# Kernel tuning notes

Measured on AMD Instinct MI355X. Metric: run time of the kernel, lower is better.

The kernel has to match this reference:

```python
import jax, jax.numpy as jnp
import numpy as np

B, S, D = 64, 512, 768   # docs, bert seq len, bert hidden
E = 32                   # entities per doc
N_ENT = B * E            # 2048 global entity segments
MPE = 4                  # mentions per entity
M = N_ENT * MPE          # 8192 flat mentions
N_TYPES = 6
P = B * E * (E - 1)      # 63488 ordered pairs (h != t), per all_possible_pair


def setup_inputs() -> dict:
    key = jax.random.key(0)
    k1, k2, k3 = jax.random.split(key, 3)
    hidden = jax.random.normal(k1, (B, S, D), dtype=jnp.float32)
    # every entity has exactly MPE mentions -> no empty segments
    mention_entity = (jnp.arange(M, dtype=jnp.int32) // MPE)
    # positions indexed at pos+1 in the original, so keep pos in [0, S-1)
    mention_pos = jax.random.randint(k2, (M,), 0, S - 1, dtype=jnp.int32)
    # all ordered pairs h != t within each doc (all_possible_pair semantics)
    idx = np.arange(E)
    hh, tt = np.meshgrid(idx, idx, indexing='ij')
    mask = hh != tt
    hh, tt = hh[mask], tt[mask]              # [E*(E-1)]
    doc = np.repeat(np.arange(B), hh.size)   # [P]
    pair_head = jnp.asarray(doc * E + np.tile(hh, B), dtype=jnp.int32)
    pair_tail = jnp.asarray(doc * E + np.tile(tt, B), dtype=jnp.int32)
    pair_doc = jnp.asarray(doc, dtype=jnp.int32)
    ent_type = jax.random.randint(k3, (N_ENT,), 0, N_TYPES, dtype=jnp.int32)
    return {
        'hidden': hidden,
        'mention_entity': mention_entity,
        'mention_pos': mention_pos,
        'pair_head': pair_head,
        'pair_tail': pair_tail,
        'pair_doc': pair_doc,
        'ent_type': ent_type,
    }


def reference(hidden, mention_entity, mention_pos, pair_head, pair_tail, pair_doc, ent_type):
    # --- aggregate_entities: ragged per-entity logsumexp over mention tokens ---
    mention_doc = mention_entity // E                      # [M]
    m_emb = hidden[mention_doc, mention_pos + 1]           # [M, D] gather (pos[0]+1)
    seg_max = jax.ops.segment_max(m_emb, mention_entity, num_segments=N_ENT)  # [N_ENT, D]
    ent = jnp.log(
        jax.ops.segment_sum(jnp.exp(m_emb - seg_max[mention_entity]),
                            mention_entity, num_segments=N_ENT)
    ) + seg_max                                            # [N_ENT, D] stable logsumexp
    # --- extract_feature: per-pair stack of [cls, ent_h, ent_t] ---
    cls = hidden[:, 0]                                     # [B, D]
    feature_set = jnp.stack(
        [cls[pair_doc], ent[pair_head], ent[pair_tail]], axis=1)  # [P, 3, D]
    # --- pair type features: one_hot(..., 6).sum over the (h, t) pair ---
    types_oh = jax.nn.one_hot(ent_type, N_TYPES, dtype=jnp.float32)  # [N_ENT, 6]
    pair_types = types_oh[pair_head] + types_oh[pair_tail]           # [P, 6]
    return feature_set, pair_types
```

## Files before the change

### kernel.cpp

```cpp
#include <hip/hip_runtime.h>

#define B 64
#define S 512
#define D 768
#define E 32
#define N_ENT (B * E)
#define MPE 4
#define M (N_ENT * MPE)
#define N_TYPES 6
#define P (B * E * (E - 1))

#define D4 (D / 4)
#define LSE_THREADS (N_ENT * D4)
#define LSE_BLOCKS (LSE_THREADS / 256)
#define TYPES_ELEMS (P * N_TYPES)
#define TYPES_BLOCKS ((TYPES_ELEMS + 255) / 256)
#define FEAT_SLOTS (P * 3 * D4)

typedef float f32x4 __attribute__((ext_vector_type(4)));

__device__ __forceinline__ float lse4(float a, float b, float c, float d) {
    float mx = fmaxf(fmaxf(a, b), fmaxf(c, d));
    return logf(expf(a - mx) + expf(b - mx) + expf(c - mx) + expf(d - mx)) + mx;
}

__global__ __launch_bounds__(256) void prep_kernel(
    const float* __restrict__ hidden,
    const int* __restrict__ mention_entity,
    const int* __restrict__ mention_pos,
    const int* __restrict__ pair_head,
    const int* __restrict__ pair_tail,
    const int* __restrict__ ent_type,
    float* __restrict__ ent,
    float* __restrict__ out_types) {
    const unsigned b = blockIdx.x;
    const unsigned t = threadIdx.x;

    if (b < LSE_BLOCKS) {
        const unsigned idx = b * 256u + t;
        const unsigned e = idx / D4;
        const unsigned d4 = idx - e * D4;
        const int doc = mention_entity[e * MPE] / E;
        const float* rowbase = hidden + (size_t)doc * S * D + (size_t)d4 * 4;

        f32x4 x[MPE];
#pragma unroll
        for (int m = 0; m < MPE; ++m) {
            const int pos = mention_pos[e * MPE + m] + 1;
            x[m] = *(const f32x4*)(rowbase + (size_t)pos * D);
        }
        f32x4 o;
        o.x = lse4(x[0].x, x[1].x, x[2].x, x[3].x);
        o.y = lse4(x[0].y, x[1].y, x[2].y, x[3].y);
        o.z = lse4(x[0].z, x[1].z, x[2].z, x[3].z);
        o.w = lse4(x[0].w, x[1].w, x[2].w, x[3].w);
        *(f32x4*)(ent + (size_t)e * D + (size_t)d4 * 4) = o;
    } else {
        const unsigned i = (b - LSE_BLOCKS) * 256u + t;
        if (i < TYPES_ELEMS) {
            const unsigned p = i / N_TYPES;
            const int ty = (int)(i - p * N_TYPES);
            const int th = ent_type[pair_head[p]];
            const int tt = ent_type[pair_tail[p]];
            out_types[i] = (float)((ty == th) + (ty == tt));
        }
    }
}

__global__ __launch_bounds__(256) void feat_kernel(
    const float* __restrict__ hidden,
    const int* __restrict__ pair_head,
    const int* __restrict__ pair_tail,
    const int* __restrict__ pair_doc,
    const float* __restrict__ ent,
    f32x4* __restrict__ out4) {
    const unsigned stride = gridDim.x * blockDim.x;
    for (unsigned idx = blockIdx.x * blockDim.x + threadIdx.x;
         idx < (unsigned)FEAT_SLOTS; idx += stride) {
        const unsigned p = idx / (3 * D4);
        const unsigned rem = idx - p * (3 * D4);
        const unsigned r = rem / D4;
        const unsigned d4 = rem - r * D4;

        const f32x4* src;
        if (r == 0) {
            src = (const f32x4*)(hidden + (size_t)pair_doc[p] * (S * D));
        } else {
            const int q = (r == 1) ? pair_head[p] : pair_tail[p];
            src = (const f32x4*)(ent + (size_t)q * D);
        }
        __builtin_nontemporal_store(src[d4], &out4[idx]);
    }
}

extern "C" void kernel_launch(void* const* d_in, const int* in_sizes, int n_in,
                              void* d_out, int out_size, void* d_ws, size_t ws_size,
                              hipStream_t stream) {
    const float* hidden       = (const float*)d_in[0];
    const int* mention_entity = (const int*)d_in[1];
    const int* mention_pos    = (const int*)d_in[2];
    const int* pair_head      = (const int*)d_in[3];
    const int* pair_tail      = (const int*)d_in[4];
    const int* pair_doc       = (const int*)d_in[5];
    const int* ent_type       = (const int*)d_in[6];

    float* out       = (float*)d_out;
    float* out_feat  = out;
    float* out_types = out + (size_t)P * 3 * D;

    float* ent = (float*)d_ws;

    prep_kernel<<<LSE_BLOCKS + TYPES_BLOCKS, 256, 0, stream>>>(
        hidden, mention_entity, mention_pos, pair_head, pair_tail, ent_type,
        ent, out_types);

    feat_kernel<<<2048, 256, 0, stream>>>(
        hidden, pair_head, pair_tail, pair_doc, ent, (f32x4*)out_feat);
}
```

Measured before the change: 104.0 us.

## Move CLS row copy into prep kernel to overlap with entity logsumexp

Splits the feature-writing work so the CLS slice of each pair row, which does not depend on entity embeddings, is written by extra blocks in the first kernel alongside the logsumexp and type work. The second kernel then writes only the head and tail entity slices. The aim is to move about a third of the output traffic earlier so it overlaps with the prep phase and shortens the dependent second kernel. Writes now land in strided sub-rows rather than fully contiguous 3*D rows, which may reduce store coalescing at row boundaries.

```diff
diff --git a/kernel.cpp b/kernel.cpp
--- a/kernel.cpp
+++ b/kernel.cpp
@@ -11,11 +11,13 @@
 #define P (B * E * (E - 1))
 
 #define D4 (D / 4)
-#define LSE_THREADS (N_ENT * D4)
-#define LSE_BLOCKS (LSE_THREADS / 256)
+#define LSE_BLOCKS (N_ENT * D4 / 256)
 #define TYPES_ELEMS (P * N_TYPES)
 #define TYPES_BLOCKS ((TYPES_ELEMS + 255) / 256)
-#define FEAT_SLOTS (P * 3 * D4)
+#define CLS_BASE (LSE_BLOCKS + TYPES_BLOCKS)
+#define CLS_GRID 2048
+#define CLS_SLOTS (P * D4)
+#define HT_SLOTS (P * 2 * D4)
 
 typedef float f32x4 __attribute__((ext_vector_type(4)));
 
@@ -24,14 +26,16 @@
     return logf(expf(a - mx) + expf(b - mx) + expf(c - mx) + expf(d - mx)) + mx;
 }
 
-__global__ __launch_bounds__(256) void prep_kernel(
+__global__ __launch_bounds__(256) void prep_cls_kernel(
     const float* __restrict__ hidden,
     const int* __restrict__ mention_entity,
     const int* __restrict__ mention_pos,
     const int* __restrict__ pair_head,
     const int* __restrict__ pair_tail,
+    const int* __restrict__ pair_doc,
     const int* __restrict__ ent_type,
     float* __restrict__ ent,
+    float* __restrict__ out_feat,
     float* __restrict__ out_types) {
     const unsigned b = blockIdx.x;
     const unsigned t = threadIdx.x;
@@ -55,7 +59,7 @@
         o.z = lse4(x[0].z, x[1].z, x[2].z, x[3].z);
         o.w = lse4(x[0].w, x[1].w, x[2].w, x[3].w);
         *(f32x4*)(ent + (size_t)e * D + (size_t)d4 * 4) = o;
-    } else {
+    } else if (b < CLS_BASE) {
         const unsigned i = (b - LSE_BLOCKS) * 256u + t;
         if (i < TYPES_ELEMS) {
             const unsigned p = i / N_TYPES;
@@ -64,32 +68,35 @@
             const int tt = ent_type[pair_tail[p]];
             out_types[i] = (float)((ty == th) + (ty == tt));
         }
+    } else {
+        f32x4* out4 = (f32x4*)out_feat;
+        const unsigned stride = CLS_GRID * 256u;
+        for (unsigned idx = (b - CLS_BASE) * 256u + t; idx < (unsigned)CLS_SLOTS;
+             idx += stride) {
+            const unsigned p = idx / D4;
+            const unsigned d4 = idx - p * D4;
+            const f32x4* src = (const f32x4*)(hidden + (size_t)pair_doc[p] * (S * D));
+            __builtin_nontemporal_store(src[d4], &out4[(size_t)p * (3 * D4) + d4]);
+        }
     }
 }
 
-__global__ __launch_bounds__(256) void feat_kernel(
-    const float* __restrict__ hidden,
+__global__ __launch_bounds__(256) void ht_kernel(
     const int* __restrict__ pair_head,
     const int* __restrict__ pair_tail,
-    const int* __restrict__ pair_doc,
     const float* __restrict__ ent,
     f32x4* __restrict__ out4) {
     const unsigned stride = gridDim.x * blockDim.x;
     for (unsigned idx = blockIdx.x * blockDim.x + threadIdx.x;
-         idx < (unsigned)FEAT_SLOTS; idx += stride) {
-        const unsigned p = idx / (3 * D4);
-        const unsigned rem = idx - p * (3 * D4);
+         idx < (unsigned)HT_SLOTS; idx += stride) {
+        const unsigned p = idx / (2 * D4);
+        const unsigned rem = idx - p * (2 * D4);
         const unsigned r = rem / D4;
         const unsigned d4 = rem - r * D4;
-
-        const f32x4* src;
-        if (r == 0) {
-            src = (const f32x4*)(hidden + (size_t)pair_doc[p] * (S * D));
-        } else {
-            const int q = (r == 1) ? pair_head[p] : pair_tail[p];
-            src = (const f32x4*)(ent + (size_t)q * D);
-        }
-        __builtin_nontemporal_store(src[d4], &out4[idx]);
+        const int q = (r == 0) ? pair_head[p] : pair_tail[p];
+        const f32x4* src = (const f32x4*)(ent + (size_t)q * D);
+        __builtin_nontemporal_store(
+            src[d4], &out4[(size_t)p * (3 * D4) + (size_t)(r + 1) * D4 + d4]);
     }
 }
 
@@ -110,10 +117,10 @@
 
     float* ent = (float*)d_ws;
 
-    prep_kernel<<<LSE_BLOCKS + TYPES_BLOCKS, 256, 0, stream>>>(
-        hidden, mention_entity, mention_pos, pair_head, pair_tail, ent_type,
-        ent, out_types);
+    prep_cls_kernel<<<CLS_BASE + CLS_GRID, 256, 0, stream>>>(
+        hidden, mention_entity, mention_pos, pair_head, pair_tail, pair_doc,
+        ent_type, ent, out_feat, out_types);
 
-    feat_kernel<<<2048, 256, 0, stream>>>(
-        hidden, pair_head, pair_tail, pair_doc, ent, (f32x4*)out_feat);
+    ht_kernel<<<2048, 256, 0, stream>>>(
+        pair_head, pair_tail, ent, (f32x4*)out_feat);
 }
```

New measurement: 116.2 us. 1.12x slower.

## Fuse entity logsumexp into pair feature kernel, recomputing per pair

Applied to the files above, without the earlier changes.

Merges the prep and feature kernels into one launch. Each pair slot now recomputes the entity logsumexp from the gathered mention rows instead of reading a precomputed ent buffer, and type features are spread across the same grid. This removes a kernel launch and the ent workspace round trip. In exchange, each entity's logsumexp is recomputed about 62 times, adding many exp/log operations and gathered loads to a store-bound loop.

```diff
diff --git a/kernel.cpp b/kernel.cpp
--- a/kernel.cpp
+++ b/kernel.cpp
@@ -11,11 +11,10 @@
 #define P (B * E * (E - 1))
 
 #define D4 (D / 4)
-#define LSE_THREADS (N_ENT * D4)
-#define LSE_BLOCKS (LSE_THREADS / 256)
+#define FEAT_SLOTS (P * 3 * D4)
+#define GRID 2048
 #define TYPES_ELEMS (P * N_TYPES)
-#define TYPES_BLOCKS ((TYPES_ELEMS + 255) / 256)
-#define FEAT_SLOTS (P * 3 * D4)
+#define TYPES_PER_BLOCK ((TYPES_ELEMS + GRID - 1) / GRID)
 
 typedef float f32x4 __attribute__((ext_vector_type(4)));
 
@@ -24,40 +23,22 @@
     return logf(expf(a - mx) + expf(b - mx) + expf(c - mx) + expf(d - mx)) + mx;
 }
 
-__global__ __launch_bounds__(256) void prep_kernel(
+__global__ __launch_bounds__(256) void fused_kernel(
     const float* __restrict__ hidden,
     const int* __restrict__ mention_entity,
     const int* __restrict__ mention_pos,
     const int* __restrict__ pair_head,
     const int* __restrict__ pair_tail,
+    const int* __restrict__ pair_doc,
     const int* __restrict__ ent_type,
-    float* __restrict__ ent,
+    f32x4* __restrict__ out4,
     float* __restrict__ out_types) {
     const unsigned b = blockIdx.x;
     const unsigned t = threadIdx.x;
 
-    if (b < LSE_BLOCKS) {
-        const unsigned idx = b * 256u + t;
-        const unsigned e = idx / D4;
-        const unsigned d4 = idx - e * D4;
-        const int doc = mention_entity[e * MPE] / E;
-        const float* rowbase = hidden + (size_t)doc * S * D + (size_t)d4 * 4;
-
-        f32x4 x[MPE];
-#pragma unroll
-        for (int m = 0; m < MPE; ++m) {
-            const int pos = mention_pos[e * MPE + m] + 1;
-            x[m] = *(const f32x4*)(rowbase + (size_t)pos * D);
-        }
-        f32x4 o;
-        o.x = lse4(x[0].x, x[1].x, x[2].x, x[3].x);
-        o.y = lse4(x[0].y, x[1].y, x[2].y, x[3].y);
-        o.z = lse4(x[0].z, x[1].z, x[2].z, x[3].z);
-        o.w = lse4(x[0].w, x[1].w, x[2].w, x[3].w);
-        *(f32x4*)(ent + (size_t)e * D + (size_t)d4 * 4) = o;
-    } else {
-        const unsigned i = (b - LSE_BLOCKS) * 256u + t;
-        if (i < TYPES_ELEMS) {
+    {
+        const unsigned i = b * TYPES_PER_BLOCK + t;
+        if (t < TYPES_PER_BLOCK && i < (unsigned)TYPES_ELEMS) {
             const unsigned p = i / N_TYPES;
             const int ty = (int)(i - p * N_TYPES);
             const int th = ent_type[pair_head[p]];
@@ -65,31 +46,36 @@
             out_types[i] = (float)((ty == th) + (ty == tt));
         }
     }
-}
 
-__global__ __launch_bounds__(256) void feat_kernel(
-    const float* __restrict__ hidden,
-    const int* __restrict__ pair_head,
-    const int* __restrict__ pair_tail,
-    const int* __restrict__ pair_doc,
-    const float* __restrict__ ent,
-    f32x4* __restrict__ out4) {
-    const unsigned stride = gridDim.x * blockDim.x;
-    for (unsigned idx = blockIdx.x * blockDim.x + threadIdx.x;
-         idx < (unsigned)FEAT_SLOTS; idx += stride) {
+    const unsigned stride = GRID * 256u;
+    for (unsigned idx = b * 256u + t; idx < (unsigned)FEAT_SLOTS; idx += stride) {
         const unsigned p = idx / (3 * D4);
         const unsigned rem = idx - p * (3 * D4);
         const unsigned r = rem / D4;
         const unsigned d4 = rem - r * D4;
 
-        const f32x4* src;
+        f32x4 v;
         if (r == 0) {
-            src = (const f32x4*)(hidden + (size_t)pair_doc[p] * (S * D));
+            const f32x4* cls4 =
+                (const f32x4*)(hidden + (size_t)pair_doc[p] * (S * D));
+            v = cls4[d4];
         } else {
             const int q = (r == 1) ? pair_head[p] : pair_tail[p];
-            src = (const f32x4*)(ent + (size_t)q * D);
+            const int mbase = q * MPE;
+            const int doc = mention_entity[mbase] / E;
+            const float* rowbase = hidden + (size_t)doc * S * D + (size_t)d4 * 4;
+            f32x4 x[MPE];
+#pragma unroll
+            for (int m = 0; m < MPE; ++m) {
+                const int pos = mention_pos[mbase + m] + 1;
+                x[m] = *(const f32x4*)(rowbase + (size_t)pos * D);
+            }
+            v.x = lse4(x[0].x, x[1].x, x[2].x, x[3].x);
+            v.y = lse4(x[0].y, x[1].y, x[2].y, x[3].y);
+            v.z = lse4(x[0].z, x[1].z, x[2].z, x[3].z);
+            v.w = lse4(x[0].w, x[1].w, x[2].w, x[3].w);
         }
-        __builtin_nontemporal_store(src[d4], &out4[idx]);
+        __builtin_nontemporal_store(v, &out4[idx]);
     }
 }
 
@@ -105,15 +91,9 @@
     const int* ent_type       = (const int*)d_in[6];
 
     float* out       = (float*)d_out;
-    float* out_feat  = out;
     float* out_types = out + (size_t)P * 3 * D;
 
-    float* ent = (float*)d_ws;
-
-    prep_kernel<<<LSE_BLOCKS + TYPES_BLOCKS, 256, 0, stream>>>(
-        hidden, mention_entity, mention_pos, pair_head, pair_tail, ent_type,
-        ent, out_types);
-
-    feat_kernel<<<2048, 256, 0, stream>>>(
-        hidden, pair_head, pair_tail, pair_doc, ent, (f32x4*)out_feat);
+    fused_kernel<<<GRID, 256, 0, stream>>>(
+        hidden, mention_entity, mention_pos, pair_head, pair_tail, pair_doc,
+        ent_type, (f32x4*)out, out_types);
 }
```

Result: slower. 252.3 us (+142.5%).
